# Performance work log

Measured on AMD Instinct MI355X. Metric: run time of the kernel, lower is better.

Reference implementation:

```python
import jax, jax.numpy as jnp
import numpy as np

SM_SCALE = 1.0 / np.sqrt(64.0)  # 1/sqrt(dim_qk)


def setup_inputs() -> dict:
    key = jax.random.key(0)
    k1, k2, k3 = jax.random.split(key, 3)
    B, S, H, Hkv, Dqk, Dv = 1, 4096, 8, 2, 64, 64
    q = jax.random.normal(k1, (B, S, H, Dqk), dtype=jnp.float32)
    k = jax.random.normal(k2, (B, S, Hkv, Dqk), dtype=jnp.float32)
    v = jax.random.normal(k3, (B, S, Hkv, Dv), dtype=jnp.float32)
    return {"q": q, "k": k, "v": v}


def reference(q, k, v):
    # q: [B,S,H,Dqk], k: [B,S,Hkv,Dqk], v: [B,S,Hkv,Dv]; query head h uses kv head h // groups
    B, S, H, Dqk = q.shape
    Hkv = k.shape[2]
    G = H // Hkv  # groups per kv head
    k_exp = jnp.repeat(k, G, axis=2)  # [B,S,H,Dqk], head h -> kv head h//G
    v_exp = jnp.repeat(v, G, axis=2)  # [B,S,H,Dv]
    scores = jnp.einsum('bqhd,bkhd->bhqk', q, k_exp) * SM_SCALE  # [B,H,S,S]
    # causal mask: query i attends to keys j <= i
    qi = jnp.arange(S)[:, None]
    kj = jnp.arange(S)[None, :]
    scores = jnp.where(qi >= kj, scores, -jnp.inf)
    p = jax.nn.softmax(scores, axis=-1)  # online-softmax result, computed densely
    out = jnp.einsum('bhqk,bkhd->bqhd', p, v_exp)  # [B,S,H,Dv]
    return out
```

## Files before the change

### kernel.cpp

```cpp
#include <hip/hip_runtime.h>
#include <hip/hip_bf16.h>

typedef __attribute__((ext_vector_type(8))) __bf16 bf16x8;
typedef __attribute__((ext_vector_type(4))) __bf16 bf16x4;
typedef __attribute__((ext_vector_type(2))) __bf16 bf16x2;
typedef __attribute__((ext_vector_type(4))) float f32x4;
typedef __attribute__((ext_vector_type(16))) float f32x16;
typedef __attribute__((ext_vector_type(2))) int i32x2;

constexpr int S_LEN = 4096;
constexpr int H = 8;
constexpr int HKV = 2;
constexpr int D = 64;
constexpr int BK = 64;
constexpr int QW = 32;
constexpr int WAVES = 4;
constexpr int QB_ROWS = QW * WAVES;
constexpr int NQB = S_LEN / QB_ROWS;
constexpr int NKT = S_LEN / BK;
constexpr float QSCALE = 0.125f * 1.44269504088896f;

__device__ __forceinline__ float fexp2(float x) {
  return __builtin_amdgcn_exp2f(x);
}

__device__ __forceinline__ int swz(int row, int col) {
  return (row * 64 + col) ^ ((((row >> 2) ^ row) & 7) << 3);
}

#define GLOAD_LDS16(g, l)                                        \
  __builtin_amdgcn_global_load_lds(                              \
      (const __attribute__((address_space(1))) void*)(g),        \
      (__attribute__((address_space(3))) void*)(l), 16, 0, 0)

__device__ __forceinline__ bf16x8 load8_scaled(const float* p, float scale) {
  f32x4 a = *reinterpret_cast<const f32x4*>(p);
  f32x4 b = *reinterpret_cast<const f32x4*>(p + 4);
  bf16x8 r;
  r[0] = (__bf16)(a[0] * scale); r[1] = (__bf16)(a[1] * scale);
  r[2] = (__bf16)(a[2] * scale); r[3] = (__bf16)(a[3] * scale);
  r[4] = (__bf16)(b[0] * scale); r[5] = (__bf16)(b[1] * scale);
  r[6] = (__bf16)(b[2] * scale); r[7] = (__bf16)(b[3] * scale);
  return r;
}

__device__ __forceinline__ int pk2(float lo, float hi) {
  bf16x2 t;
  t[0] = (__bf16)lo;
  t[1] = (__bf16)hi;
  return __builtin_bit_cast(int, t);
}

__global__ __launch_bounds__(256) void pack_kv_kernel(
    const float* __restrict__ k, const float* __restrict__ v,
    __bf16* __restrict__ kp, __bf16* __restrict__ vp) {
  const int tid  = threadIdx.x;
  const int tile = blockIdx.x & (NKT - 1);
  const int hkv  = blockIdx.x >> 6;
  const int kv0  = tile * BK;
  __bf16* kb = kp + (size_t)(hkv * NKT + tile) * 4096;
  __bf16* vb = vp + (size_t)(hkv * NKT + tile) * 4096;
  {
    const int row = tid >> 2, cg = (tid & 3) * 16;
    const float* src = k + ((size_t)(kv0 + row) * HKV + hkv) * D + cg;
    bf16x8 w0, w1;
#pragma unroll
    for (int j = 0; j < 8; ++j) w0[j] = (__bf16)src[j];
#pragma unroll
    for (int j = 0; j < 8; ++j) w1[j] = (__bf16)src[8 + j];
    *reinterpret_cast<bf16x8*>(&kb[swz(row, cg)]) = w0;
    *reinterpret_cast<bf16x8*>(&kb[swz(row, cg + 8)]) = w1;
  }
  {
    const int s16 = tid >> 4, s4 = (tid & 15) * 4;
    f32x4 lv[4];
#pragma unroll
    for (int u = 0; u < 4; ++u)
      lv[u] = *reinterpret_cast<const f32x4*>(
          v + ((size_t)(kv0 + s16 * 4 + u) * HKV + hkv) * D + s4);
#pragma unroll
    for (int j = 0; j < 4; ++j) {
      bf16x4 vw;
      vw[0] = (__bf16)lv[0][j]; vw[1] = (__bf16)lv[1][j];
      vw[2] = (__bf16)lv[2][j]; vw[3] = (__bf16)lv[3][j];
      *reinterpret_cast<bf16x4*>(&vb[swz(s4 + j, s16 * 4)]) = vw;
    }
  }
}

template <int LOG2C, bool SPLIT, bool PACKED>
__global__ __launch_bounds__(256, 2) void gqa_fwd_kernel(
    const float* __restrict__ q, const float* __restrict__ k,
    const float* __restrict__ v, float* __restrict__ out,
    const __bf16* __restrict__ kp, const __bf16* __restrict__ vp,
    __bf16* __restrict__ po, float* __restrict__ ml) {
  constexpr int TPC = (1 << LOG2C) / BK;

  const int tid  = threadIdx.x;
  const int lane = tid & 63;
  const int wid  = tid >> 6;
  const int cl   = lane & 31;
  const int hi   = lane >> 5;

  const int hp   = blockIdx.x & 3;
  const int h0   = hp * 2;
  const int widx = blockIdx.x >> 2;
  int qb = 0, c = 0;
  {
    int acc0 = 0;
    for (int qx = NQB - 1; qx >= 0; --qx) {
      const int n = ((qx * QB_ROWS + QB_ROWS - 1) >> LOG2C) + 1;
      if (widx < acc0 + n) { qb = qx; c = widx - acc0; break; }
      acc0 += n;
    }
  }
  const int cmax = (qb * QB_ROWS + QB_ROWS - 1) >> LOG2C;
  const int hkv = hp >> 1;
  const int q0w = qb * QB_ROWS + wid * QW;
  const int nt  = (c < cmax) ? TPC : ((QB_ROWS / BK) * (qb + 1) - TPC * cmax);
  const int kb0 = c << LOG2C;
  const int qq  = q0w + cl;

  __shared__ __bf16 klds[2][64 * 64];
  __shared__ __bf16 vlds[2][64 * 64];

  bf16x8 qf[2][4];
#pragma unroll
  for (int hd = 0; hd < 2; ++hd)
#pragma unroll
    for (int s = 0; s < 4; ++s)
      qf[hd][s] = load8_scaled(
          q + ((size_t)qq * H + h0 + hd) * D + s * 16 + hi * 8, QSCALE);

  float l_[2] = {0.f, 0.f};
  f32x16 oa[2][2];
#pragma unroll
  for (int hd = 0; hd < 2; ++hd)
#pragma unroll
    for (int dt = 0; dt < 2; ++dt)
#pragma unroll
      for (int e = 0; e < 16; ++e) oa[hd][dt][e] = 0.f;

  const int s16 = tid >> 4;
  const int s4  = (tid & 15) * 4;
  auto stage = [&](int buf, int t) {
    if constexpr (PACKED) {
      const size_t blob = (size_t)(hkv * NKT + (kb0 >> 6) + t) * 4096;
      const char* kg = (const char*)(kp + blob) + wid * 2048 + (lane << 4);
      const char* vg = (const char*)(vp + blob) + wid * 2048 + (lane << 4);
      char* kl = (char*)&klds[buf][0] + wid * 2048;
      char* vl = (char*)&vlds[buf][0] + wid * 2048;
      GLOAD_LDS16(kg, kl);
      GLOAD_LDS16(kg + 1024, kl + 1024);
      GLOAD_LDS16(vg, vl);
      GLOAD_LDS16(vg + 1024, vl + 1024);
    } else {
      const int kb = kb0 + t * BK;
#pragma unroll
      for (int u = 0; u < 4; ++u) {
        f32x4 ka = *reinterpret_cast<const f32x4*>(
            k + ((size_t)(kb + u * 16 + s16) * HKV + hkv) * D + s4);
        bf16x4 kw;
        kw[0] = (__bf16)ka[0]; kw[1] = (__bf16)ka[1];
        kw[2] = (__bf16)ka[2]; kw[3] = (__bf16)ka[3];
        *reinterpret_cast<bf16x4*>(&klds[buf][swz(u * 16 + s16, s4)]) = kw;
      }
      f32x4 lv[4];
#pragma unroll
      for (int u = 0; u < 4; ++u)
        lv[u] = *reinterpret_cast<const f32x4*>(
            v + ((size_t)(kb + s16 * 4 + u) * HKV + hkv) * D + s4);
#pragma unroll
      for (int j = 0; j < 4; ++j) {
        bf16x4 vw;
        vw[0] = (__bf16)lv[0][j]; vw[1] = (__bf16)lv[1][j];
        vw[2] = (__bf16)lv[2][j]; vw[3] = (__bf16)lv[3][j];
        *reinterpret_cast<bf16x4*>(&vlds[buf][swz(s4 + j, s16 * 4)]) = vw;
      }
    }
  };

  auto tile_body = [&](int buf, int t) {
    const int kb = kb0 + t * BK;
    if (kb > q0w + 31) return;

    f32x16 st[2][2];
#pragma unroll
    for (int hd = 0; hd < 2; ++hd)
#pragma unroll
      for (int kt = 0; kt < 2; ++kt)
#pragma unroll
        for (int e = 0; e < 16; ++e) st[hd][kt][e] = 0.f;
    __builtin_amdgcn_s_setprio(1);
#pragma unroll
    for (int s = 0; s < 4; ++s) {
      bf16x8 kf0 = *reinterpret_cast<const bf16x8*>(
          &klds[buf][swz(cl, s * 16 + hi * 8)]);
      bf16x8 kf1 = *reinterpret_cast<const bf16x8*>(
          &klds[buf][swz(32 + cl, s * 16 + hi * 8)]);
      st[0][0] = __builtin_amdgcn_mfma_f32_32x32x16_bf16(kf0, qf[0][s], st[0][0], 0, 0, 0);
      st[0][1] = __builtin_amdgcn_mfma_f32_32x32x16_bf16(kf1, qf[0][s], st[0][1], 0, 0, 0);
      st[1][0] = __builtin_amdgcn_mfma_f32_32x32x16_bf16(kf0, qf[1][s], st[1][0], 0, 0, 0);
      st[1][1] = __builtin_amdgcn_mfma_f32_32x32x16_bf16(kf1, qf[1][s], st[1][1], 0, 0, 0);
    }
    __builtin_amdgcn_s_setprio(0);

    if (kb + 63 > q0w) {
#pragma unroll
      for (int kt = 0; kt < 2; ++kt)
#pragma unroll
        for (int rr = 0; rr < 16; ++rr) {
          const int key = kb + 32 * kt + (rr & 3) + 8 * (rr >> 2) + 4 * hi;
          if (key > qq) { st[0][kt][rr] = -1e30f; st[1][kt][rr] = -1e30f; }
        }
    }

#pragma unroll
    for (int hd = 0; hd < 2; ++hd) {
      float ps0 = 0.f, ps1 = 0.f;
#pragma unroll
      for (int kt = 0; kt < 2; ++kt)
#pragma unroll
        for (int e = 0; e < 8; ++e) {
          const float pa = fexp2(st[hd][kt][e]);
          const float pb = fexp2(st[hd][kt][8 + e]);
          ps0 += pa; ps1 += pb;
          st[hd][kt][e] = pa; st[hd][kt][8 + e] = pb;
        }
      l_[hd] += ps0 + ps1;
    }

    __builtin_amdgcn_s_setprio(1);
#pragma unroll
    for (int s = 0; s < 4; ++s) {
      const int kt = s >> 1;
      const int g  = (s & 1) * 2;
      bf16x8 vf0 = *reinterpret_cast<const bf16x8*>(
          &vlds[buf][swz(cl, s * 16 + hi * 8)]);
      bf16x8 vf1 = *reinterpret_cast<const bf16x8*>(
          &vlds[buf][swz(32 + cl, s * 16 + hi * 8)]);
#pragma unroll
      for (int hd = 0; hd < 2; ++hd) {
        const int x0 = pk2(st[hd][kt][4 * g + 0], st[hd][kt][4 * g + 1]);
        const int x1 = pk2(st[hd][kt][4 * g + 2], st[hd][kt][4 * g + 3]);
        const int y0 = pk2(st[hd][kt][4 * g + 4], st[hd][kt][4 * g + 5]);
        const int y1 = pk2(st[hd][kt][4 * g + 6], st[hd][kt][4 * g + 7]);
        i32x2 w0 = __builtin_amdgcn_permlane32_swap(x0, y0, false, false);
        i32x2 w1 = __builtin_amdgcn_permlane32_swap(x1, y1, false, false);
        int pu[4];
        pu[0] = w0[0]; pu[1] = w1[0]; pu[2] = w0[1]; pu[3] = w1[1];
        bf16x8 pf;
        memcpy(&pf, pu, 16);
        oa[hd][0] = __builtin_amdgcn_mfma_f32_32x32x16_bf16(vf0, pf, oa[hd][0], 0, 0, 0);
        oa[hd][1] = __builtin_amdgcn_mfma_f32_32x32x16_bf16(vf1, pf, oa[hd][1], 0, 0, 0);
      }
    }
    __builtin_amdgcn_s_setprio(0);
  };

  stage(0, 0);
  __syncthreads();

  for (int t = 0; t < nt; t += 2) {
    if (t + 1 < nt) stage(1, t + 1);
    tile_body(0, t);
    __syncthreads();
    if (t + 2 < nt) stage(0, t + 2);
    tile_body(1, t + 1);
    __syncthreads();
  }

#pragma unroll
  for (int hd = 0; hd < 2; ++hd) {
    const float lsum = l_[hd] + __shfl_xor(l_[hd], 32, 64);
    const int h = h0 + hd;
    if (SPLIT && cmax > 0) {
      __bf16* prow = po + ((size_t)(c * S_LEN + qq) * H + h) * D;
#pragma unroll
      for (int dt = 0; dt < 2; ++dt)
#pragma unroll
        for (int qd = 0; qd < 4; ++qd) {
          bf16x4 pb;
          pb[0] = (__bf16)oa[hd][dt][4 * qd + 0]; pb[1] = (__bf16)oa[hd][dt][4 * qd + 1];
          pb[2] = (__bf16)oa[hd][dt][4 * qd + 2]; pb[3] = (__bf16)oa[hd][dt][4 * qd + 3];
          *reinterpret_cast<bf16x4*>(prow + dt * 32 + qd * 8 + hi * 4) = pb;
        }
      if (lane < 32) ml[(size_t)(c * S_LEN + qq) * H + h] = lsum;
    } else {
      const float inv = 1.0f / lsum;
      float* orow = out + ((size_t)qq * H + h) * D;
#pragma unroll
      for (int dt = 0; dt < 2; ++dt)
#pragma unroll
        for (int qd = 0; qd < 4; ++qd) {
          f32x4 o;
          o[0] = oa[hd][dt][4 * qd + 0] * inv; o[1] = oa[hd][dt][4 * qd + 1] * inv;
          o[2] = oa[hd][dt][4 * qd + 2] * inv; o[3] = oa[hd][dt][4 * qd + 3] * inv;
          *reinterpret_cast<f32x4*>(orow + dt * 32 + qd * 8 + hi * 4) = o;
        }
    }
  }
}

template <int LOG2C>
__global__ __launch_bounds__(256) void combine_kernel(
    const __bf16* __restrict__ po, const float* __restrict__ ml,
    float* __restrict__ out) {
  const int tid = threadIdx.x;
  const int rl  = tid >> 3;
  const int d0  = (tid & 7) * 8;
  const int h   = blockIdx.x & 7;
  const int row = (1 << LOG2C) + (blockIdx.x >> 3) * 32 + rl;
  const int cmax = row >> LOG2C;

  float lsum = 0.f;
  float osum[8];
#pragma unroll
  for (int j = 0; j < 8; ++j) osum[j] = 0.f;
  for (int cc = 0; cc <= cmax; ++cc) {
    const size_t base = (size_t)(cc * S_LEN + row) * H + h;
    lsum += ml[base];
    bf16x8 pv = *reinterpret_cast<const bf16x8*>(po + base * D + d0);
#pragma unroll
    for (int j = 0; j < 8; ++j) osum[j] += (float)pv[j];
  }
  const float inv = 1.0f / lsum;
  float* orow = out + ((size_t)row * H + h) * D + d0;
  f32x4 o0, o1;
  o0[0] = osum[0] * inv; o0[1] = osum[1] * inv;
  o0[2] = osum[2] * inv; o0[3] = osum[3] * inv;
  o1[0] = osum[4] * inv; o1[1] = osum[5] * inv;
  o1[2] = osum[6] * inv; o1[3] = osum[7] * inv;
  *reinterpret_cast<f32x4*>(orow) = o0;
  *reinterpret_cast<f32x4*>(orow + 4) = o1;
}

static int nwork_items(int log2c) {
  int s = 0;
  for (int qb = 0; qb < NQB; ++qb)
    s += ((qb * QB_ROWS + QB_ROWS - 1) >> log2c) + 1;
  return s;
}

extern "C" void kernel_launch(void* const* d_in, const int* in_sizes, int n_in,
                              void* d_out, int out_size, void* d_ws, size_t ws_size,
                              hipStream_t stream) {
  const float* q = (const float*)d_in[0];
  const float* k = (const float*)d_in[1];
  const float* v = (const float*)d_in[2];
  float* out = (float*)d_out;

  const size_t pack_e = (size_t)S_LEN * HKV * D;
  const size_t po8 = 8ull * S_LEN * H * D, ml8 = 8ull * S_LEN * H;
  const size_t po4 = 4ull * S_LEN * H * D, ml4 = 4ull * S_LEN * H;
  const size_t pack_b = pack_e * 2 * sizeof(__bf16);

  __bf16* kp = (__bf16*)d_ws;
  __bf16* vp = kp + pack_e;
  char* rest = (char*)d_ws + pack_b;

  if (ws_size >= pack_b + po8 * 2 + ml8 * 4) {
    __bf16* po = (__bf16*)rest;
    float* mlp = (float*)(rest + po8 * 2);
    pack_kv_kernel<<<dim3(HKV * NKT), dim3(256), 0, stream>>>(k, v, kp, vp);
    gqa_fwd_kernel<9, true, true><<<dim3(4 * nwork_items(9)), dim3(256), 0, stream>>>(
        q, k, v, out, kp, vp, po, mlp);
    combine_kernel<9><<<dim3((S_LEN - 512) / 32 * 8), dim3(256), 0, stream>>>(po, mlp, out);
  } else if (ws_size >= pack_b + po4 * 2 + ml4 * 4) {
    __bf16* po = (__bf16*)rest;
    float* mlp = (float*)(rest + po4 * 2);
    pack_kv_kernel<<<dim3(HKV * NKT), dim3(256), 0, stream>>>(k, v, kp, vp);
    gqa_fwd_kernel<10, true, true><<<dim3(4 * nwork_items(10)), dim3(256), 0, stream>>>(
        q, k, v, out, kp, vp, po, mlp);
    combine_kernel<10><<<dim3((S_LEN - 1024) / 32 * 8), dim3(256), 0, stream>>>(po, mlp, out);
  } else if (ws_size >= pack_b) {
    pack_kv_kernel<<<dim3(HKV * NKT), dim3(256), 0, stream>>>(k, v, kp, vp);
    gqa_fwd_kernel<12, false, true><<<dim3(4 * nwork_items(12)), dim3(256), 0, stream>>>(
        q, k, v, out, kp, vp, nullptr, nullptr);
  } else {
    gqa_fwd_kernel<12, false, false><<<dim3(4 * nwork_items(12)), dim3(256), 0, stream>>>(
        q, k, v, out, nullptr, nullptr, nullptr, nullptr);
  }
}
```

Measured before the change: 52.34 us.

## Finer KV split, per-head kernel variants, and vectorized two-block KV packing

```diff
diff --git a/kernel.cpp b/kernel.cpp
--- a/kernel.cpp
+++ b/kernel.cpp
@@ -55,46 +55,45 @@
     const float* __restrict__ k, const float* __restrict__ v,
     __bf16* __restrict__ kp, __bf16* __restrict__ vp) {
   const int tid  = threadIdx.x;
-  const int tile = blockIdx.x & (NKT - 1);
-  const int hkv  = blockIdx.x >> 6;
+  const int sb   = blockIdx.x & 1;
+  const int tile = (blockIdx.x >> 1) & (NKT - 1);
+  const int hkv  = blockIdx.x >> 7;
   const int kv0  = tile * BK;
   __bf16* kb = kp + (size_t)(hkv * NKT + tile) * 4096;
   __bf16* vb = vp + (size_t)(hkv * NKT + tile) * 4096;
   {
-    const int row = tid >> 2, cg = (tid & 3) * 16;
+    const int row = sb * 32 + (tid >> 3), cg = (tid & 7) * 8;
     const float* src = k + ((size_t)(kv0 + row) * HKV + hkv) * D + cg;
-    bf16x8 w0, w1;
-#pragma unroll
-    for (int j = 0; j < 8; ++j) w0[j] = (__bf16)src[j];
-#pragma unroll
-    for (int j = 0; j < 8; ++j) w1[j] = (__bf16)src[8 + j];
-    *reinterpret_cast<bf16x8*>(&kb[swz(row, cg)]) = w0;
-    *reinterpret_cast<bf16x8*>(&kb[swz(row, cg + 8)]) = w1;
+    f32x4 a = *reinterpret_cast<const f32x4*>(src);
+    f32x4 b = *reinterpret_cast<const f32x4*>(src + 4);
+    bf16x8 w;
+    w[0] = (__bf16)a[0]; w[1] = (__bf16)a[1]; w[2] = (__bf16)a[2]; w[3] = (__bf16)a[3];
+    w[4] = (__bf16)b[0]; w[5] = (__bf16)b[1]; w[6] = (__bf16)b[2]; w[7] = (__bf16)b[3];
+    *reinterpret_cast<bf16x8*>(&kb[swz(row, cg)]) = w;
   }
   {
-    const int s16 = tid >> 4, s4 = (tid & 15) * 4;
-    f32x4 lv[4];
-#pragma unroll
-    for (int u = 0; u < 4; ++u)
-      lv[u] = *reinterpret_cast<const f32x4*>(
-          v + ((size_t)(kv0 + s16 * 4 + u) * HKV + hkv) * D + s4);
+    const int kvl = sb * 32 + (tid >> 4) * 2, d0 = (tid & 15) * 4;
+    f32x4 lv0 = *reinterpret_cast<const f32x4*>(
+        v + ((size_t)(kv0 + kvl) * HKV + hkv) * D + d0);
+    f32x4 lv1 = *reinterpret_cast<const f32x4*>(
+        v + ((size_t)(kv0 + kvl + 1) * HKV + hkv) * D + d0);
 #pragma unroll
     for (int j = 0; j < 4; ++j) {
-      bf16x4 vw;
-      vw[0] = (__bf16)lv[0][j]; vw[1] = (__bf16)lv[1][j];
-      vw[2] = (__bf16)lv[2][j]; vw[3] = (__bf16)lv[3][j];
-      *reinterpret_cast<bf16x4*>(&vb[swz(s4 + j, s16 * 4)]) = vw;
-    }
-  }
-}
-
-template <int LOG2C, bool SPLIT, bool PACKED>
-__global__ __launch_bounds__(256, 2) void gqa_fwd_kernel(
+      bf16x2 vw;
+      vw[0] = (__bf16)lv0[j]; vw[1] = (__bf16)lv1[j];
+      *reinterpret_cast<bf16x2*>(&vb[swz(d0 + j, kvl)]) = vw;
+    }
+  }
+}
+
+template <int LOG2C, int NH, bool SPLIT, bool PACKED>
+__global__ __launch_bounds__(256, NH == 1 ? 3 : 2) void gqa_fwd_kernel(
     const float* __restrict__ q, const float* __restrict__ k,
     const float* __restrict__ v, float* __restrict__ out,
     const __bf16* __restrict__ kp, const __bf16* __restrict__ vp,
     __bf16* __restrict__ po, float* __restrict__ ml) {
   constexpr int TPC = (1 << LOG2C) / BK;
+  constexpr int NHG = H / NH;
 
   const int tid  = threadIdx.x;
   const int lane = tid & 63;
@@ -102,9 +101,9 @@
   const int cl   = lane & 31;
   const int hi   = lane >> 5;
 
-  const int hp   = blockIdx.x & 3;
-  const int h0   = hp * 2;
-  const int widx = blockIdx.x >> 2;
+  const int hg   = blockIdx.x % NHG;
+  const int h0   = hg * NH;
+  const int widx = blockIdx.x / NHG;
   int qb = 0, c = 0;
   {
     int acc0 = 0;
@@ -115,7 +114,7 @@
     }
   }
   const int cmax = (qb * QB_ROWS + QB_ROWS - 1) >> LOG2C;
-  const int hkv = hp >> 1;
+  const int hkv = h0 >> 2;
   const int q0w = qb * QB_ROWS + wid * QW;
   const int nt  = (c < cmax) ? TPC : ((QB_ROWS / BK) * (qb + 1) - TPC * cmax);
   const int kb0 = c << LOG2C;
@@ -124,22 +123,24 @@
   __shared__ __bf16 klds[2][64 * 64];
   __shared__ __bf16 vlds[2][64 * 64];
 
-  bf16x8 qf[2][4];
-#pragma unroll
-  for (int hd = 0; hd < 2; ++hd)
+  bf16x8 qf[NH][4];
+#pragma unroll
+  for (int hd = 0; hd < NH; ++hd)
 #pragma unroll
     for (int s = 0; s < 4; ++s)
       qf[hd][s] = load8_scaled(
           q + ((size_t)qq * H + h0 + hd) * D + s * 16 + hi * 8, QSCALE);
 
-  float l_[2] = {0.f, 0.f};
-  f32x16 oa[2][2];
-#pragma unroll
-  for (int hd = 0; hd < 2; ++hd)
+  float l_[NH];
+  f32x16 oa[NH][2];
+#pragma unroll
+  for (int hd = 0; hd < NH; ++hd) {
+    l_[hd] = 0.f;
 #pragma unroll
     for (int dt = 0; dt < 2; ++dt)
 #pragma unroll
       for (int e = 0; e < 16; ++e) oa[hd][dt][e] = 0.f;
+  }
 
   const int s16 = tid >> 4;
   const int s4  = (tid & 15) * 4;
@@ -184,9 +185,9 @@
     const int kb = kb0 + t * BK;
     if (kb > q0w + 31) return;
 
-    f32x16 st[2][2];
-#pragma unroll
-    for (int hd = 0; hd < 2; ++hd)
+    f32x16 st[NH][2];
+#pragma unroll
+    for (int hd = 0; hd < NH; ++hd)
 #pragma unroll
       for (int kt = 0; kt < 2; ++kt)
 #pragma unroll
@@ -198,10 +199,11 @@
           &klds[buf][swz(cl, s * 16 + hi * 8)]);
       bf16x8 kf1 = *reinterpret_cast<const bf16x8*>(
           &klds[buf][swz(32 + cl, s * 16 + hi * 8)]);
-      st[0][0] = __builtin_amdgcn_mfma_f32_32x32x16_bf16(kf0, qf[0][s], st[0][0], 0, 0, 0);
-      st[0][1] = __builtin_amdgcn_mfma_f32_32x32x16_bf16(kf1, qf[0][s], st[0][1], 0, 0, 0);
-      st[1][0] = __builtin_amdgcn_mfma_f32_32x32x16_bf16(kf0, qf[1][s], st[1][0], 0, 0, 0);
-      st[1][1] = __builtin_amdgcn_mfma_f32_32x32x16_bf16(kf1, qf[1][s], st[1][1], 0, 0, 0);
+#pragma unroll
+      for (int hd = 0; hd < NH; ++hd) {
+        st[hd][0] = __builtin_amdgcn_mfma_f32_32x32x16_bf16(kf0, qf[hd][s], st[hd][0], 0, 0, 0);
+        st[hd][1] = __builtin_amdgcn_mfma_f32_32x32x16_bf16(kf1, qf[hd][s], st[hd][1], 0, 0, 0);
+      }
     }
     __builtin_amdgcn_s_setprio(0);
 
@@ -211,12 +213,15 @@
 #pragma unroll
         for (int rr = 0; rr < 16; ++rr) {
           const int key = kb + 32 * kt + (rr & 3) + 8 * (rr >> 2) + 4 * hi;
-          if (key > qq) { st[0][kt][rr] = -1e30f; st[1][kt][rr] = -1e30f; }
+          if (key > qq) {
+#pragma unroll
+            for (int hd = 0; hd < NH; ++hd) st[hd][kt][rr] = -1e30f;
+          }
         }
     }
 
 #pragma unroll
-    for (int hd = 0; hd < 2; ++hd) {
+    for (int hd = 0; hd < NH; ++hd) {
       float ps0 = 0.f, ps1 = 0.f;
 #pragma unroll
       for (int kt = 0; kt < 2; ++kt)
@@ -240,7 +245,7 @@
       bf16x8 vf1 = *reinterpret_cast<const bf16x8*>(
           &vlds[buf][swz(32 + cl, s * 16 + hi * 8)]);
 #pragma unroll
-      for (int hd = 0; hd < 2; ++hd) {
+      for (int hd = 0; hd < NH; ++hd) {
         const int x0 = pk2(st[hd][kt][4 * g + 0], st[hd][kt][4 * g + 1]);
         const int x1 = pk2(st[hd][kt][4 * g + 2], st[hd][kt][4 * g + 3]);
         const int y0 = pk2(st[hd][kt][4 * g + 4], st[hd][kt][4 * g + 5]);
@@ -271,7 +276,7 @@
   }
 
 #pragma unroll
-  for (int hd = 0; hd < 2; ++hd) {
+  for (int hd = 0; hd < NH; ++hd) {
     const float lsum = l_[hd] + __shfl_xor(l_[hd], 32, 64);
     const int h = h0 + hd;
     if (SPLIT && cmax > 0) {
@@ -351,34 +356,42 @@
   float* out = (float*)d_out;
 
   const size_t pack_e = (size_t)S_LEN * HKV * D;
-  const size_t po8 = 8ull * S_LEN * H * D, ml8 = 8ull * S_LEN * H;
-  const size_t po4 = 4ull * S_LEN * H * D, ml4 = 4ull * S_LEN * H;
   const size_t pack_b = pack_e * 2 * sizeof(__bf16);
+  auto po_e = [](int ns) { return (size_t)ns * S_LEN * H * D; };
+  auto ml_e = [](int ns) { return (size_t)ns * S_LEN * H; };
 
   __bf16* kp = (__bf16*)d_ws;
   __bf16* vp = kp + pack_e;
   char* rest = (char*)d_ws + pack_b;
-
-  if (ws_size >= pack_b + po8 * 2 + ml8 * 4) {
+  const int npack = 2 * HKV * NKT;
+
+  if (ws_size >= pack_b + po_e(16) * 2 + ml_e(16) * 4) {
     __bf16* po = (__bf16*)rest;
-    float* mlp = (float*)(rest + po8 * 2);
-    pack_kv_kernel<<<dim3(HKV * NKT), dim3(256), 0, stream>>>(k, v, kp, vp);
-    gqa_fwd_kernel<9, true, true><<<dim3(4 * nwork_items(9)), dim3(256), 0, stream>>>(
+    float* mlp = (float*)(rest + po_e(16) * 2);
+    pack_kv_kernel<<<dim3(npack), dim3(256), 0, stream>>>(k, v, kp, vp);
+    gqa_fwd_kernel<8, 2, true, true><<<dim3(4 * nwork_items(8)), dim3(256), 0, stream>>>(
+        q, k, v, out, kp, vp, po, mlp);
+    combine_kernel<8><<<dim3((S_LEN - 256) / 32 * 8), dim3(256), 0, stream>>>(po, mlp, out);
+  } else if (ws_size >= pack_b + po_e(8) * 2 + ml_e(8) * 4) {
+    __bf16* po = (__bf16*)rest;
+    float* mlp = (float*)(rest + po_e(8) * 2);
+    pack_kv_kernel<<<dim3(npack), dim3(256), 0, stream>>>(k, v, kp, vp);
+    gqa_fwd_kernel<9, 1, true, true><<<dim3(8 * nwork_items(9)), dim3(256), 0, stream>>>(
         q, k, v, out, kp, vp, po, mlp);
     combine_kernel<9><<<dim3((S_LEN - 512) / 32 * 8), dim3(256), 0, stream>>>(po, mlp, out);
-  } else if (ws_size >= pack_b + po4 * 2 + ml4 * 4) {
+  } else if (ws_size >= pack_b + po_e(4) * 2 + ml_e(4) * 4) {
     __bf16* po = (__bf16*)rest;
-    float* mlp = (float*)(rest + po4 * 2);
-    pack_kv_kernel<<<dim3(HKV * NKT), dim3(256), 0, stream>>>(k, v, kp, vp);
-    gqa_fwd_kernel<10, true, true><<<dim3(4 * nwork_items(10)), dim3(256), 0, stream>>>(
+    float* mlp = (float*)(rest + po_e(4) * 2);
+    pack_kv_kernel<<<dim3(npack), dim3(256), 0, stream>>>(k, v, kp, vp);
+    gqa_fwd_kernel<10, 1, true, true><<<dim3(8 * nwork_items(10)), dim3(256), 0, stream>>>(
         q, k, v, out, kp, vp, po, mlp);
     combine_kernel<10><<<dim3((S_LEN - 1024) / 32 * 8), dim3(256), 0, stream>>>(po, mlp, out);
   } else if (ws_size >= pack_b) {
-    pack_kv_kernel<<<dim3(HKV * NKT), dim3(256), 0, stream>>>(k, v, kp, vp);
-    gqa_fwd_kernel<12, false, true><<<dim3(4 * nwork_items(12)), dim3(256), 0, stream>>>(
+    pack_kv_kernel<<<dim3(npack), dim3(256), 0, stream>>>(k, v, kp, vp);
+    gqa_fwd_kernel<12, 1, false, true><<<dim3(8 * nwork_items(12)), dim3(256), 0, stream>>>(
         q, k, v, out, kp, vp, nullptr, nullptr);
   } else {
-    gqa_fwd_kernel<12, false, false><<<dim3(4 * nwork_items(12)), dim3(256), 0, stream>>>(
+    gqa_fwd_kernel<12, 1, false, false><<<dim3(8 * nwork_items(12)), dim3(256), 0, stream>>>(
         q, k, v, out, nullptr, nullptr, nullptr, nullptr);
   }
 }
```

Result: slower. 57.77 us (+10.4%).
